# Kernel tuning notes

Hardware: AMD Instinct MI355X
Metric: run time of the kernel (lower is better)

The kernel has to match this reference:

```python
import jax, jax.numpy as jnp
import numpy as np

B, S, D_MODEL, D_Q = 16, 2048, 384, 64


def setup_inputs() -> dict:
    key = jax.random.key(0)
    k1, k2, k3, k4 = jax.random.split(key, 4)
    x = jax.random.normal(k1, (B, S, D_MODEL), dtype=jnp.float32)
    # nn.Linear(d_model, d_q, bias=False) weights, stored as [d_model, d_q] so q = x @ Wq
    scale = 1.0 / np.sqrt(D_MODEL)
    Wq = jax.random.normal(k2, (D_MODEL, D_Q), dtype=jnp.float32) * scale
    Wk = jax.random.normal(k3, (D_MODEL, D_Q), dtype=jnp.float32) * scale
    Wv = jax.random.normal(k4, (D_MODEL, D_Q), dtype=jnp.float32) * scale
    return {"x": x, "Wq": Wq, "Wk": Wk, "Wv": Wv}


def reference(x, Wq, Wk, Wv):
    # x: [B, S, d_model]
    q = jnp.einsum("bsd,de->bse", x, Wq)  # [B, S, d_q]
    k = jnp.einsum("bsd,de->bse", x, Wk)
    v = jnp.einsum("bsd,de->bse", x, Wv)
    d_q = q.shape[-1]
    # full S x S score matrix, scaled by sqrt(d_q) as in the torch code (k.size(-1)**0.5)
    scores = jnp.einsum("bse,bte->bst", q, k) / jnp.sqrt(jnp.float32(d_q))
    s = x.shape[1]
    causal = jnp.tril(jnp.ones((s, s), dtype=bool))  # [S, S]
    scores = jnp.where(causal, scores, jnp.float32(-jnp.inf))
    probs = jax.nn.softmax(scores, axis=-1)
    # dropout is identity in eval/reference mode
    out = jnp.einsum("bst,bte->bse", probs, v)  # [B, S, d_q]
    return out
```

## Files before the change

### kernel.cpp

```cpp
#include <hip/hip_runtime.h>
#include <hip/hip_bf16.h>
#include <math.h>

#define BB 16
#define SS 2048
#define DM 384
#define DQ 64
#define M_ROWS (BB * SS)

typedef short short8 __attribute__((ext_vector_type(8)));
typedef float f32x4  __attribute__((ext_vector_type(4)));

#define WT_OFF 0
#define QB_OFF 73728
#define KB_OFF (QB_OFF + M_ROWS * DQ)
#define VT_OFF (KB_OFF + M_ROWS * DQ)

#define QSCALE 0.18033688011112042f

__device__ __forceinline__ short f2bf(float f) {
  unsigned u = __builtin_bit_cast(unsigned, f);
  unsigned r = (u + 0x7fffu + ((u >> 16) & 1u)) >> 16;
  return (short)r;
}
__device__ __forceinline__ unsigned pack2bf(float a, float b) {
  return (unsigned)(unsigned short)f2bf(a) |
         ((unsigned)(unsigned short)f2bf(b) << 16);
}
__device__ __forceinline__ void async16(const short* g, short* l) {
  __builtin_amdgcn_global_load_lds(
      (const __attribute__((address_space(1))) unsigned int*)g,
      (__attribute__((address_space(3))) unsigned int*)l, 16, 0, 0);
}

__global__ void prep_w_kernel(const float* __restrict__ Wq,
                              const float* __restrict__ Wk,
                              const float* __restrict__ Wv,
                              short* __restrict__ ws) {
  int o = blockIdx.x * 256 + threadIdx.x;
  int mat = o / (DM * DQ);
  int r = o % (DM * DQ);
  int k = r / DQ, n = r % DQ;
  const float* W = (mat == 0) ? Wq : (mat == 1) ? Wk : Wv;
  ws[WT_OFF + mat * (DM * DQ) + n * DM + k] = f2bf(W[k * DQ + n]);
}

__global__ __launch_bounds__(256) void qkv_proj_mfma(
    const float* __restrict__ x, const short* __restrict__ ws_r,
    short* __restrict__ ws_w) {
  __shared__ short Wtc[192 * 64];
  __shared__ short Ep[64 * 200];
  const int tid = threadIdx.x;
  const int lane = tid & 63, w = tid >> 6;
  const int cidx = lane & 15, g = lane >> 4;
  const int g8 = g * 8, g4 = g * 4;
  const int sw7 = cidx & 7;
  const int rows0 = blockIdx.x * 64;
  const short* Wt = ws_r + WT_OFF;

  f32x4 acc[12];
  #pragma unroll
  for (int i = 0; i < 12; ++i) acc[i] = (f32x4){0.f, 0.f, 0.f, 0.f};

  const float* xr = x + (size_t)(rows0 + 16 * w + cidx) * DM;

  for (int k0 = 0; k0 < DM; k0 += 64) {
    float4 xa0 = *(const float4*)(xr + k0 + g8);
    float4 xa1 = *(const float4*)(xr + k0 + g8 + 4);
    float4 xb0 = *(const float4*)(xr + k0 + 32 + g8);
    float4 xb1 = *(const float4*)(xr + k0 + 32 + g8 + 4);
    __syncthreads();
    #pragma unroll
    for (int it = 0; it < 6; ++it) {
      int i = it * 256 + tid;
      int row = i >> 3, gr = i & 7;
      const short* src = Wt + row * DM + k0 + ((gr ^ (row & 7)) * 8);
      async16(src, &Wtc[(it * 256 + w * 64) * 8]);
    }
    __syncthreads();

    short8 a0, a1;
    a0[0]=f2bf(xa0.x); a0[1]=f2bf(xa0.y); a0[2]=f2bf(xa0.z); a0[3]=f2bf(xa0.w);
    a0[4]=f2bf(xa1.x); a0[5]=f2bf(xa1.y); a0[6]=f2bf(xa1.z); a0[7]=f2bf(xa1.w);
    a1[0]=f2bf(xb0.x); a1[1]=f2bf(xb0.y); a1[2]=f2bf(xb0.z); a1[3]=f2bf(xb0.w);
    a1[4]=f2bf(xb1.x); a1[5]=f2bf(xb1.y); a1[6]=f2bf(xb1.z); a1[7]=f2bf(xb1.w);

    #pragma unroll
    for (int ct = 0; ct < 12; ++ct) {
      int row = ct * 16 + cidx;
      short8 b0 = *(const short8*)&Wtc[row * 64 + ((g ^ sw7) * 8)];
      short8 b1 = *(const short8*)&Wtc[row * 64 + (((g + 4) ^ sw7) * 8)];
      acc[ct] = __builtin_amdgcn_mfma_f32_16x16x32_bf16(a0, b0, acc[ct], 0, 0, 0);
      acc[ct] = __builtin_amdgcn_mfma_f32_16x16x32_bf16(a1, b1, acc[ct], 0, 0, 0);
    }
  }

  __syncthreads();
  const int erow = 16 * w + g4;
  #pragma unroll
  for (int ct = 0; ct < 4; ++ct)
    #pragma unroll
    for (int r = 0; r < 4; ++r) {
      Ep[(erow + r) * 200 + ct * 16 + cidx]       = f2bf(acc[ct][r] * QSCALE);
      Ep[(erow + r) * 200 + 64 + ct * 16 + cidx]  = f2bf(acc[4 + ct][r]);
      Ep[(ct * 16 + cidx) * 200 + 128 + erow + r] = f2bf(acc[8 + ct][r]);
    }
  __syncthreads();

  short* Qb = ws_w + QB_OFF;
  short* Kb = ws_w + KB_OFF;
  short* Vt = ws_w + VT_OFF;
  const int bidx = rows0 >> 11;
  const int srow0 = rows0 & 2047;
  #pragma unroll
  for (int t2 = 0; t2 < 2; ++t2) {
    int i = t2 * 256 + tid;
    int row = i >> 3, gq = i & 7;
    *(short8*)&Qb[(size_t)(rows0 + row) * DQ + gq * 8] =
        *(const short8*)&Ep[row * 200 + gq * 8];
    *(short8*)&Kb[(size_t)(rows0 + row) * DQ + gq * 8] =
        *(const short8*)&Ep[row * 200 + 64 + gq * 8];
    *(short8*)&Vt[(size_t)bidx * (64 * SS) + (size_t)row * SS + srow0 + gq * 8] =
        *(const short8*)&Ep[row * 200 + 128 + gq * 8];
  }
}

__global__ __launch_bounds__(256, 4) void flash_mfma(
    const short* __restrict__ ws, float* __restrict__ O) {
  __shared__ short smem[20480];
  short* Ks  = smem;
  short* Vts = smem + 8192;
  const int b = blockIdx.y;
  const int qt = (b < 8) ? (63 - (int)blockIdx.x) : (int)blockIdx.x;
  const int q0 = qt * 32;
  const int tid = threadIdx.x;
  const int lane = tid & 63, w = tid >> 6;
  const int qg = w & 1, s = w >> 1;
  const int cidx = lane & 15, g = lane >> 4;
  const int g8 = g * 8, g4 = g * 4;
  const int sw7 = cidx & 7;
  short* Ps = smem + 16384 + w * 1024;

  const short* Qb = ws + QB_OFF + (size_t)b * SS * DQ;
  const short* Kb = ws + KB_OFF + (size_t)b * SS * DQ;
  const short* Vt = ws + VT_OFF + (size_t)b * 64 * SS;

  const int qrow = q0 + qg * 16;
  const int qglob = qrow + cidx;
  short8 qf0 = *(const short8*)&Qb[(size_t)qglob * DQ + g8];
  short8 qf1 = *(const short8*)&Qb[(size_t)qglob * DQ + 32 + g8];

  f32x4 o[4];
  #pragma unroll
  for (int i = 0; i < 4; ++i) o[i] = (f32x4){0.f, 0.f, 0.f, 0.f};
  float l = 0.f;

  const int ktmax = qt >> 1;
  const int nss = (ktmax + 2) >> 1;
  for (int ssi = 0; ssi < nss; ++ssi) {
    const int kbase = ssi * 128;
    __syncthreads();
    #pragma unroll
    for (int t4 = 0; t4 < 4; ++t4) {
      int i = t4 * 256 + tid;
      int row = i >> 3, gr = i & 7;
      async16(Kb + (size_t)(kbase + row) * DQ + ((gr ^ (row & 7)) * 8),
              &Ks[(t4 * 256 + w * 64) * 8]);
    }
    #pragma unroll
    for (int t4 = 0; t4 < 4; ++t4) {
      int i = t4 * 256 + tid;
      int row = i >> 4, gr = i & 15;
      async16(Vt + (size_t)row * SS + kbase + ((gr ^ (row & 15)) * 8),
              &Vts[(t4 * 256 + w * 64) * 8]);
    }
    __syncthreads();

    const int kt64 = ssi * 2 + s;
    if (kt64 <= ktmax) {
      f32x4 sc[4];
      #pragma unroll
      for (int ct = 0; ct < 4; ++ct) {
        int krow = s * 64 + ct * 16 + cidx;
        short8 kf0 = *(const short8*)&Ks[krow * 64 + ((g ^ sw7) * 8)];
        short8 kf1 = *(const short8*)&Ks[krow * 64 + (((g + 4) ^ sw7) * 8)];
        f32x4 a = (f32x4){0.f, 0.f, 0.f, 0.f};
        a = __builtin_amdgcn_mfma_f32_16x16x32_bf16(kf0, qf0, a, 0, 0, 0);
        a = __builtin_amdgcn_mfma_f32_16x16x32_bf16(kf1, qf1, a, 0, 0, 0);
        sc[ct] = a;
      }
      if (kt64 == ktmax) {
        #pragma unroll
        for (int ct = 0; ct < 4; ++ct) {
          int key = kbase + s * 64 + ct * 16 + g4;
          #pragma unroll
          for (int r = 0; r < 4; ++r)
            if (key + r > qglob) sc[ct][r] = -1e30f;
        }
      }
      #pragma unroll
      for (int ct = 0; ct < 4; ++ct) {
        #pragma unroll
        for (int r = 0; r < 4; ++r) {
          float p = __builtin_amdgcn_exp2f(sc[ct][r]);
          sc[ct][r] = p;
          l += p;
        }
        int gb = ct * 2 + (g >> 1);
        uint2 pk;
        pk.x = pack2bf(sc[ct][0], sc[ct][1]);
        pk.y = pack2bf(sc[ct][2], sc[ct][3]);
        *(uint2*)&Ps[cidx * 64 + ((gb ^ sw7) * 8) + (g & 1) * 4] = pk;
      }
      #pragma unroll
      for (int ks = 0; ks < 2; ++ks) {
        short8 pf = *(const short8*)&Ps[cidx * 64 + (((ks * 4 + g) ^ sw7) * 8)];
        #pragma unroll
        for (int dt = 0; dt < 4; ++dt) {
          int vrow = dt * 16 + cidx;
          short8 vf = *(const short8*)
              &Vts[vrow * 128 + (((s * 8 + ks * 4 + g) ^ cidx) * 8)];
          o[dt] = __builtin_amdgcn_mfma_f32_16x16x32_bf16(vf, pf, o[dt], 0, 0, 0);
        }
      }
    }
  }

  l += __shfl_xor(l, 16);
  l += __shfl_xor(l, 32);

  float* o1x = (float*)smem;
  float* l1x = (float*)(smem + 4096);
  float* Of  = (float*)(smem + 4224);
  __syncthreads();
  if (s == 1) {
    int base = qg * 1024;
    #pragma unroll
    for (int dt = 0; dt < 4; ++dt)
      #pragma unroll
      for (int r = 0; r < 4; ++r)
        o1x[base + dt * 256 + r * 64 + lane] = o[dt][r];
    if (g == 0) l1x[qg * 16 + cidx] = l;
  }
  __syncthreads();
  if (s == 0) {
    int base = qg * 1024;
    float inv = 1.0f / (l + l1x[qg * 16 + cidx]);
    #pragma unroll
    for (int dt = 0; dt < 4; ++dt)
      #pragma unroll
      for (int r = 0; r < 4; ++r)
        Of[(qg * 16 + cidx) * 72 + dt * 16 + g4 + r] =
            (o[dt][r] + o1x[base + dt * 256 + r * 64 + lane]) * inv;
  }
  __syncthreads();
  #pragma unroll
  for (int t2 = 0; t2 < 2; ++t2) {
    int i = t2 * 256 + tid;
    int qb = i >> 4, f4 = i & 15;
    float4 v = *(const float4*)&Of[qb * 72 + f4 * 4];
    *(float4*)&O[((size_t)b * SS + q0 + qb) * DQ + f4 * 4] = v;
  }
}

extern "C" void kernel_launch(void* const* d_in, const int* in_sizes, int n_in,
                              void* d_out, int out_size, void* d_ws, size_t ws_size,
                              hipStream_t stream) {
  const float* x  = (const float*)d_in[0];
  const float* Wq = (const float*)d_in[1];
  const float* Wk = (const float*)d_in[2];
  const float* Wv = (const float*)d_in[3];
  short* ws = (short*)d_ws;
  float* out = (float*)d_out;

  prep_w_kernel<<<288, 256, 0, stream>>>(Wq, Wk, Wv, ws);
  qkv_proj_mfma<<<M_ROWS / 64, 256, 0, stream>>>(x, ws, ws);
  flash_mfma<<<dim3(64, BB), 256, 0, stream>>>(ws, out);
}
```

Measured before the change: 126.6 us.

## Double-buffer W tiles in projection and K/V tiles in flash attention

The QKV projection now double-buffers weight tiles in LDS and prefetches the next x chunk while the current chunk's MFMAs run. The flash kernel shrinks its per-iteration key tile from 128 to 64 keys, double-buffers K/V in LDS with async prefetch of the next tile, and drops one barrier per iteration. The P scratch layout is also changed to a padded, unswizzled layout. The intent is to hide global-to-LDS load latency behind compute, at the cost of more loop iterations with less work each.

```diff
diff --git a/kernel.cpp b/kernel.cpp
--- a/kernel.cpp
+++ b/kernel.cpp
@@ -48,7 +48,7 @@
 __global__ __launch_bounds__(256) void qkv_proj_mfma(
     const float* __restrict__ x, const short* __restrict__ ws_r,
     short* __restrict__ ws_w) {
-  __shared__ short Wtc[192 * 64];
+  __shared__ short Wtc[2][12288];
   __shared__ short Ep[64 * 200];
   const int tid = threadIdx.x;
   const int lane = tid & 63, w = tid >> 6;
@@ -58,41 +58,57 @@
   const int rows0 = blockIdx.x * 64;
   const short* Wt = ws_r + WT_OFF;
 
+  const int prow = tid >> 3;
+  const int pgr = tid & 7;
+  const short* wsrc = Wt + (size_t)prow * DM + ((pgr ^ (prow & 7)) * 8);
+
   f32x4 acc[12];
   #pragma unroll
   for (int i = 0; i < 12; ++i) acc[i] = (f32x4){0.f, 0.f, 0.f, 0.f};
 
   const float* xr = x + (size_t)(rows0 + 16 * w + cidx) * DM;
 
-  for (int k0 = 0; k0 < DM; k0 += 64) {
-    float4 xa0 = *(const float4*)(xr + k0 + g8);
-    float4 xa1 = *(const float4*)(xr + k0 + g8 + 4);
-    float4 xb0 = *(const float4*)(xr + k0 + 32 + g8);
-    float4 xb1 = *(const float4*)(xr + k0 + 32 + g8 + 4);
+  float4 xc0 = *(const float4*)(xr + g8);
+  float4 xc1 = *(const float4*)(xr + g8 + 4);
+  float4 xc2 = *(const float4*)(xr + 32 + g8);
+  float4 xc3 = *(const float4*)(xr + 32 + g8 + 4);
+  #pragma unroll
+  for (int itr = 0; itr < 6; ++itr)
+    async16(wsrc + (size_t)itr * 32 * DM, &Wtc[0][(itr * 256 + w * 64) * 8]);
+
+  #pragma unroll
+  for (int it = 0; it < 6; ++it) {
     __syncthreads();
-    #pragma unroll
-    for (int it = 0; it < 6; ++it) {
-      int i = it * 256 + tid;
-      int row = i >> 3, gr = i & 7;
-      const short* src = Wt + row * DM + k0 + ((gr ^ (row & 7)) * 8);
-      async16(src, &Wtc[(it * 256 + w * 64) * 8]);
-    }
-    __syncthreads();
+
+    float4 xn0, xn1, xn2, xn3;
+    if (it < 5) {
+      const int k0n = (it + 1) * 64;
+      #pragma unroll
+      for (int itr = 0; itr < 6; ++itr)
+        async16(wsrc + (size_t)itr * 32 * DM + k0n,
+                &Wtc[(it + 1) & 1][(itr * 256 + w * 64) * 8]);
+      xn0 = *(const float4*)(xr + k0n + g8);
+      xn1 = *(const float4*)(xr + k0n + g8 + 4);
+      xn2 = *(const float4*)(xr + k0n + 32 + g8);
+      xn3 = *(const float4*)(xr + k0n + 32 + g8 + 4);
+    }
 
     short8 a0, a1;
-    a0[0]=f2bf(xa0.x); a0[1]=f2bf(xa0.y); a0[2]=f2bf(xa0.z); a0[3]=f2bf(xa0.w);
-    a0[4]=f2bf(xa1.x); a0[5]=f2bf(xa1.y); a0[6]=f2bf(xa1.z); a0[7]=f2bf(xa1.w);
-    a1[0]=f2bf(xb0.x); a1[1]=f2bf(xb0.y); a1[2]=f2bf(xb0.z); a1[3]=f2bf(xb0.w);
-    a1[4]=f2bf(xb1.x); a1[5]=f2bf(xb1.y); a1[6]=f2bf(xb1.z); a1[7]=f2bf(xb1.w);
-
+    a0[0]=f2bf(xc0.x); a0[1]=f2bf(xc0.y); a0[2]=f2bf(xc0.z); a0[3]=f2bf(xc0.w);
+    a0[4]=f2bf(xc1.x); a0[5]=f2bf(xc1.y); a0[6]=f2bf(xc1.z); a0[7]=f2bf(xc1.w);
+    a1[0]=f2bf(xc2.x); a1[1]=f2bf(xc2.y); a1[2]=f2bf(xc2.z); a1[3]=f2bf(xc2.w);
+    a1[4]=f2bf(xc3.x); a1[5]=f2bf(xc3.y); a1[6]=f2bf(xc3.z); a1[7]=f2bf(xc3.w);
+
+    const short* Wb = Wtc[it & 1];
     #pragma unroll
     for (int ct = 0; ct < 12; ++ct) {
       int row = ct * 16 + cidx;
-      short8 b0 = *(const short8*)&Wtc[row * 64 + ((g ^ sw7) * 8)];
-      short8 b1 = *(const short8*)&Wtc[row * 64 + (((g + 4) ^ sw7) * 8)];
+      short8 b0 = *(const short8*)&Wb[row * 64 + ((g ^ sw7) * 8)];
+      short8 b1 = *(const short8*)&Wb[row * 64 + (((g + 4) ^ sw7) * 8)];
       acc[ct] = __builtin_amdgcn_mfma_f32_16x16x32_bf16(a0, b0, acc[ct], 0, 0, 0);
       acc[ct] = __builtin_amdgcn_mfma_f32_16x16x32_bf16(a1, b1, acc[ct], 0, 0, 0);
     }
+    if (it < 5) { xc0 = xn0; xc1 = xn1; xc2 = xn2; xc3 = xn3; }
   }
 
   __syncthreads();
@@ -127,9 +143,7 @@
 
 __global__ __launch_bounds__(256, 4) void flash_mfma(
     const short* __restrict__ ws, float* __restrict__ O) {
-  __shared__ short smem[20480];
-  short* Ks  = smem;
-  short* Vts = smem + 8192;
+  __shared__ short smem[18944];
   const int b = blockIdx.y;
   const int qt = (b < 8) ? (63 - (int)blockIdx.x) : (int)blockIdx.x;
   const int q0 = qt * 32;
@@ -139,7 +153,7 @@
   const int cidx = lane & 15, g = lane >> 4;
   const int g8 = g * 8, g4 = g * 4;
   const int sw7 = cidx & 7;
-  short* Ps = smem + 16384 + w * 1024;
+  short* Ps = smem + 16384 + w * 640;
 
   const short* Qb = ws + QB_OFF + (size_t)b * SS * DQ;
   const short* Kb = ws + KB_OFF + (size_t)b * SS * DQ;
@@ -150,78 +164,85 @@
   short8 qf0 = *(const short8*)&Qb[(size_t)qglob * DQ + g8];
   short8 qf1 = *(const short8*)&Qb[(size_t)qglob * DQ + 32 + g8];
 
+  const int srow = tid >> 3;
+  const int sgr = tid & 7;
+  const int ssw = (sgr ^ (srow & 7)) * 8;
+  const short* kb0 = Kb + (size_t)srow * DQ + ssw;
+  const short* kb1 = Kb + (size_t)(srow + 32) * DQ + ssw;
+  const short* vb0 = Vt + (size_t)srow * SS + ssw;
+  const short* vb1 = Vt + (size_t)(srow + 32) * SS + ssw;
+  const int dst0 = (w * 64) * 8, dst1 = (256 + w * 64) * 8;
+
   f32x4 o[4];
   #pragma unroll
   for (int i = 0; i < 4; ++i) o[i] = (f32x4){0.f, 0.f, 0.f, 0.f};
   float l = 0.f;
 
-  const int ktmax = qt >> 1;
-  const int nss = (ktmax + 2) >> 1;
+  const int nss = (qt >> 1) + 1;
+
+  async16(kb0, &smem[dst0]);
+  async16(kb1, &smem[dst1]);
+  async16(vb0, &smem[8192 + dst0]);
+  async16(vb1, &smem[8192 + dst1]);
+
   for (int ssi = 0; ssi < nss; ++ssi) {
-    const int kbase = ssi * 128;
     __syncthreads();
-    #pragma unroll
-    for (int t4 = 0; t4 < 4; ++t4) {
-      int i = t4 * 256 + tid;
-      int row = i >> 3, gr = i & 7;
-      async16(Kb + (size_t)(kbase + row) * DQ + ((gr ^ (row & 7)) * 8),
-              &Ks[(t4 * 256 + w * 64) * 8]);
-    }
-    #pragma unroll
-    for (int t4 = 0; t4 < 4; ++t4) {
-      int i = t4 * 256 + tid;
-      int row = i >> 4, gr = i & 15;
-      async16(Vt + (size_t)row * SS + kbase + ((gr ^ (row & 15)) * 8),
-              &Vts[(t4 * 256 + w * 64) * 8]);
-    }
-    __syncthreads();
-
-    const int kt64 = ssi * 2 + s;
-    if (kt64 <= ktmax) {
-      f32x4 sc[4];
-      #pragma unroll
-      for (int ct = 0; ct < 4; ++ct) {
-        int krow = s * 64 + ct * 16 + cidx;
-        short8 kf0 = *(const short8*)&Ks[krow * 64 + ((g ^ sw7) * 8)];
-        short8 kf1 = *(const short8*)&Ks[krow * 64 + (((g + 4) ^ sw7) * 8)];
+
+    {
+      int nb = (ssi + 1) * 64;
+      if (nb > SS - 64) nb = SS - 64;
+      const int nbuf = ((ssi + 1) & 1) * 4096;
+      const size_t koff = (size_t)nb * DQ;
+      async16(kb0 + koff, &smem[nbuf + dst0]);
+      async16(kb1 + koff, &smem[nbuf + dst1]);
+      async16(vb0 + nb, &smem[8192 + nbuf + dst0]);
+      async16(vb1 + nb, &smem[8192 + nbuf + dst1]);
+    }
+
+    const int kt32 = ssi * 2 + s;
+    if (kt32 <= qt) {
+      const short* Kc = smem + (ssi & 1) * 4096;
+      const short* Vc = smem + 8192 + (ssi & 1) * 4096;
+      const int kbase = ssi * 64;
+      f32x4 sc[2];
+      #pragma unroll
+      for (int ct = 0; ct < 2; ++ct) {
+        int krow = s * 32 + ct * 16 + cidx;
+        short8 kf0 = *(const short8*)&Kc[krow * 64 + ((g ^ sw7) * 8)];
+        short8 kf1 = *(const short8*)&Kc[krow * 64 + (((g + 4) ^ sw7) * 8)];
         f32x4 a = (f32x4){0.f, 0.f, 0.f, 0.f};
         a = __builtin_amdgcn_mfma_f32_16x16x32_bf16(kf0, qf0, a, 0, 0, 0);
         a = __builtin_amdgcn_mfma_f32_16x16x32_bf16(kf1, qf1, a, 0, 0, 0);
         sc[ct] = a;
       }
-      if (kt64 == ktmax) {
+      if (kt32 == qt) {
         #pragma unroll
-        for (int ct = 0; ct < 4; ++ct) {
-          int key = kbase + s * 64 + ct * 16 + g4;
+        for (int ct = 0; ct < 2; ++ct) {
+          int key = kbase + s * 32 + ct * 16 + g4;
           #pragma unroll
           for (int r = 0; r < 4; ++r)
             if (key + r > qglob) sc[ct][r] = -1e30f;
         }
       }
       #pragma unroll
-      for (int ct = 0; ct < 4; ++ct) {
+      for (int ct = 0; ct < 2; ++ct) {
         #pragma unroll
         for (int r = 0; r < 4; ++r) {
           float p = __builtin_amdgcn_exp2f(sc[ct][r]);
           sc[ct][r] = p;
           l += p;
         }
-        int gb = ct * 2 + (g >> 1);
         uint2 pk;
         pk.x = pack2bf(sc[ct][0], sc[ct][1]);
         pk.y = pack2bf(sc[ct][2], sc[ct][3]);
-        *(uint2*)&Ps[cidx * 64 + ((gb ^ sw7) * 8) + (g & 1) * 4] = pk;
+        *(uint2*)&Ps[cidx * 40 + ct * 16 + g4] = pk;
       }
-      #pragma unroll
-      for (int ks = 0; ks < 2; ++ks) {
-        short8 pf = *(const short8*)&Ps[cidx * 64 + (((ks * 4 + g) ^ sw7) * 8)];
-        #pragma unroll
-        for (int dt = 0; dt < 4; ++dt) {
-          int vrow = dt * 16 + cidx;
-          short8 vf = *(const short8*)
-              &Vts[vrow * 128 + (((s * 8 + ks * 4 + g) ^ cidx) * 8)];
-          o[dt] = __builtin_amdgcn_mfma_f32_16x16x32_bf16(vf, pf, o[dt], 0, 0, 0);
-        }
+      short8 pf = *(const short8*)&Ps[cidx * 40 + g8];
+      #pragma unroll
+      for (int dt = 0; dt < 4; ++dt) {
+        int vrow = dt * 16 + cidx;
+        short8 vf = *(const short8*)&Vc[vrow * 64 + (((s * 4 + g) ^ sw7) * 8)];
+        o[dt] = __builtin_amdgcn_mfma_f32_16x16x32_bf16(vf, pf, o[dt], 0, 0, 0);
       }
     }
   }
```

After: 126.9 us. No clear change (+0.2%).
